# Performance work log

Measured on AMD Instinct MI355X. Metric: run time of the kernel, lower is better.

Reference implementation:

```python
import jax, jax.numpy as jnp
import numpy as np
from jax import lax

T, IMG, C_IN = 2048, 84, 4
HID = 256
NUM_OUT = 18
FEAT = 6 * 6 * 32  # 84 -> 42 -> 21 -> 11 -> 6 with stride-2 SAME convs


def setup_inputs() -> dict:
    key = jax.random.key(0)
    ks = jax.random.split(key, 8)
    d = {}
    d["x"] = jax.random.normal(ks[0], (T, IMG, IMG, C_IN), jnp.float32)
    cin = C_IN
    for i in range(4):
        d[f"conv_w{i}"] = jax.random.normal(ks[1 + i], (3, 3, cin, 32), jnp.float32) * (1.0 / np.sqrt(9 * cin))
        d[f"conv_b{i}"] = jnp.zeros((32,), jnp.float32)
        cin = 32
    d["lstm_w"] = jax.random.normal(ks[5], (FEAT + HID, 4 * HID), jnp.float32) * (1.0 / np.sqrt(FEAT + HID))
    d["lstm_b"] = jnp.zeros((4 * HID,), jnp.float32)
    d["fc_w"] = jax.random.normal(ks[6], (HID, NUM_OUT), jnp.float32) * 0.01
    d["fc_b"] = jnp.zeros((NUM_OUT,), jnp.float32)
    d["c_in"] = jnp.zeros((1, HID), jnp.float32)
    d["h_in"] = jnp.zeros((1, HID), jnp.float32)
    return d


def _conv_stack(x, ws, bs):
    dn = ("NHWC", "HWIO", "NHWC")
    for w, b in zip(ws, bs):
        x = jax.nn.elu(lax.conv_general_dilated(x, w, (2, 2), "SAME", dimension_numbers=dn) + b)
    return x.reshape(x.shape[0], -1)  # [T, FEAT]


def _lstm(feats, c0, h0, lstm_w, lstm_b):
    # BasicLSTMCell: gates [i, j, f, o], forget_bias = 1.0
    def step(carry, xt):
        c, h = carry  # [1, HID] each
        z = jnp.concatenate([xt[None, :], h], axis=1) @ lstm_w + lstm_b
        i, j, f, o = jnp.split(z, 4, axis=1)
        c = c * jax.nn.sigmoid(f + 1.0) + jax.nn.sigmoid(i) * jnp.tanh(j)
        h = jnp.tanh(c) * jax.nn.sigmoid(o)
        return (c, h), h[0]

    (_, _), hs = lax.scan(step, (c0, h0), feats)
    return hs  # [T, HID]


def reference(x, c_in, h_in,
              conv_w0, conv_b0, conv_w1, conv_b1,
              conv_w2, conv_b2, conv_w3, conv_b3,
              lstm_w, lstm_b, fc_w, fc_b):
    feats = _conv_stack(x, [conv_w0, conv_w1, conv_w2, conv_w3],
                        [conv_b0, conv_b1, conv_b2, conv_b3])
    hs = _lstm(feats, c_in, h_in, lstm_w, lstm_b)
    logits = hs @ fc_w + fc_b  # [T, NUM_OUT]
    return logits, hs
```

## Files before the change

### kernel.cpp

```cpp
#include <hip/hip_runtime.h>
#include <hip/hip_bf16.h>

__device__ inline float fsig(float x) { return 1.0f / (1.0f + __expf(-x)); }
__device__ inline float ftanh(float x) {
    float ax = fabsf(x);
    float e = __expf(-2.0f * ax);
    float r = (1.0f - e) / (1.0f + e);
    return x >= 0.0f ? r : -r;
}
__device__ inline float felu(float x) { return x > 0.0f ? x : expm1f(x); }

typedef _Float16 h2_t __attribute__((ext_vector_type(2)));

__device__ inline unsigned int packh2(float a, float b) {
    unsigned short ua = __builtin_bit_cast(unsigned short, (_Float16)a);
    unsigned short ub = __builtin_bit_cast(unsigned short, (_Float16)b);
    return (unsigned int)ua | ((unsigned int)ub << 16);
}
__device__ inline unsigned short f16bits(float a) {
    return __builtin_bit_cast(unsigned short, (_Float16)a);
}

__device__ inline float dot2acc(unsigned int w, unsigned int h, float acc) {
#if __has_builtin(__builtin_amdgcn_fdot2)
    return __builtin_amdgcn_fdot2(__builtin_bit_cast(h2_t, w), __builtin_bit_cast(h2_t, h), acc, false);
#else
    _Float16 wlo = __builtin_bit_cast(_Float16, (unsigned short)(w & 0xffff));
    _Float16 whi = __builtin_bit_cast(_Float16, (unsigned short)(w >> 16));
    _Float16 hlo = __builtin_bit_cast(_Float16, (unsigned short)(h & 0xffff));
    _Float16 hhi = __builtin_bit_cast(_Float16, (unsigned short)(h >> 16));
    return acc + (float)wlo * (float)hlo + (float)whi * (float)hhi;
#endif
}

__global__ __launch_bounds__(256) void conv0_kernel(const float* __restrict__ in,
                                                    const float* __restrict__ wg,
                                                    const float* __restrict__ bias,
                                                    unsigned short* __restrict__ out) {
    constexpr int W = 84, OW = 42, PAD = 0, WP = W + 2;
    __shared__ float in_s[3 * WP * 4];
    constexpr int NQ = 3 * WP;
    const int tid = threadIdx.x;
    const int oy = blockIdx.x;
    const int t = blockIdx.y;
    const int co = tid & 31;

    for (int q = tid; q < NQ; q += 256) {
        int ky = q / WP;
        int col = q - ky * WP;
        int iy = 2 * oy - PAD + ky;
        int ix = col - 1;
        float4 v = make_float4(0.f, 0.f, 0.f, 0.f);
        if (iy >= 0 && iy < W && ix >= 0 && ix < W)
            v = *(const float4*)&in[(((size_t)t * W + iy) * W + ix) * 4];
        *(float4*)&in_s[q * 4] = v;
    }

    float wr[9][4];
#pragma unroll
    for (int tap = 0; tap < 9; ++tap)
#pragma unroll
        for (int j = 0; j < 4; ++j) wr[tap][j] = wg[(tap * 4 + j) * 32 + co];
    __syncthreads();

    const int g = tid >> 5;
    constexpr int NOX = (OW + 7) / 8;
    float acc[NOX];
#pragma unroll
    for (int m = 0; m < NOX; ++m) acc[m] = 0.f;
#pragma unroll
    for (int ky = 0; ky < 3; ++ky)
#pragma unroll
        for (int kx = 0; kx < 3; ++kx) {
            float w0 = wr[ky * 3 + kx][0], w1 = wr[ky * 3 + kx][1];
            float w2 = wr[ky * 3 + kx][2], w3 = wr[ky * 3 + kx][3];
#pragma unroll
            for (int m = 0; m < NOX; ++m) {
                int ox = g + 8 * m;
                if (ox < OW) {
                    int cs = 2 * ox + kx - PAD + 1;
                    float4 xi = *(const float4*)&in_s[(ky * WP + cs) * 4];
                    acc[m] += xi.x * w0 + xi.y * w1 + xi.z * w2 + xi.w * w3;
                }
            }
        }
    float b = bias[co];
#pragma unroll
    for (int m = 0; m < NOX; ++m) {
        int ox = g + 8 * m;
        if (ox < OW)
            out[(((size_t)t * OW + oy) * OW + ox) * 32 + co] = f16bits(felu(acc[m] + b));
    }
}

template <int W, int OW, int PAD, bool F32OUT>
__global__ __launch_bounds__(256) void convh_kernel(const unsigned short* __restrict__ in,
                                                    const float* __restrict__ wg,
                                                    const float* __restrict__ bias,
                                                    void* __restrict__ outv) {
    constexpr int WP = W + 2;
    constexpr int OWH = (OW + 1) / 2;
    __shared__ __align__(16) unsigned short in_s[3][WP][32];
    __shared__ float zs[4][OW * 32];

    const int tid = threadIdx.x;
    const int oy = blockIdx.x;
    const int t = blockIdx.y;
    const int co = tid & 31;
    const int cig = (tid >> 5) & 3;
    const int oxh = tid >> 7;

    constexpr int NQ4 = 3 * WP * 4;
    uint4* in_s4 = reinterpret_cast<uint4*>(&in_s[0][0][0]);
    for (int q = tid; q < NQ4; q += 256) {
        int ky = q / (WP * 4);
        int rem = q - ky * (WP * 4);
        int col = rem >> 2, c4 = rem & 3;
        int iy = 2 * oy - PAD + ky;
        int ix = col - 1;
        uint4 v = make_uint4(0u, 0u, 0u, 0u);
        if (iy >= 0 && iy < W && ix >= 0 && ix < W)
            v = *(const uint4*)&in[(((size_t)t * W + iy) * W + ix) * 32 + c4 * 8];
        in_s4[q] = v;
    }

    unsigned int wr[9][4];
#pragma unroll
    for (int tap = 0; tap < 9; ++tap)
#pragma unroll
        for (int p = 0; p < 4; ++p)
            wr[tap][p] = packh2(wg[(tap * 32 + cig * 8 + 2 * p) * 32 + co],
                                wg[(tap * 32 + cig * 8 + 2 * p + 1) * 32 + co]);
    __syncthreads();

    float acc[OWH];
#pragma unroll
    for (int m = 0; m < OWH; ++m) acc[m] = 0.f;
#pragma unroll
    for (int ky = 0; ky < 3; ++ky)
#pragma unroll
        for (int kx = 0; kx < 3; ++kx) {
            unsigned int w0 = wr[ky * 3 + kx][0], w1 = wr[ky * 3 + kx][1];
            unsigned int w2 = wr[ky * 3 + kx][2], w3 = wr[ky * 3 + kx][3];
#pragma unroll
            for (int m = 0; m < OWH; ++m) {
                int ox = oxh * OWH + m;
                if (ox < OW) {
                    int cs = 2 * ox + kx - PAD + 1;
                    uint4 h8 = *(const uint4*)&in_s[ky][cs][cig * 8];
                    acc[m] = dot2acc(w0, h8.x, acc[m]);
                    acc[m] = dot2acc(w1, h8.y, acc[m]);
                    acc[m] = dot2acc(w2, h8.z, acc[m]);
                    acc[m] = dot2acc(w3, h8.w, acc[m]);
                }
            }
        }
#pragma unroll
    for (int m = 0; m < OWH; ++m) {
        int ox = oxh * OWH + m;
        if (ox < OW) zs[cig][ox * 32 + co] = acc[m];
    }
    __syncthreads();

    for (int idx = tid; idx < OW * 32; idx += 256) {
        float s = zs[0][idx] + zs[1][idx] + zs[2][idx] + zs[3][idx] + bias[idx & 31];
        s = felu(s);
        if constexpr (F32OUT)
            ((float*)outv)[(((size_t)t * OW + oy) * OW) * 32 + idx] = s;
        else
            ((unsigned short*)outv)[(((size_t)t * OW + oy) * OW) * 32 + idx] = f16bits(s);
    }
}

__global__ void gemm_kernel(const float* __restrict__ A, const float* __restrict__ Wx,
                            const float* __restrict__ bias, float* __restrict__ C) {
    __shared__ float As[32][64];
    __shared__ float Bs[32][64];
    const int bn = blockIdx.x, bm = blockIdx.y;
    const int tx = threadIdx.x, ty = threadIdx.y;
    const int tid = ty * 16 + tx;
    float acc[4][4] = {};
    for (int k0 = 0; k0 < 1152; k0 += 32) {
        {
            int r = tid >> 3;
            int c = (tid & 7) * 4;
            float4 a0 = *(const float4*)&A[(size_t)(bm * 64 + r) * 1152 + k0 + c];
            float4 a1 = *(const float4*)&A[(size_t)(bm * 64 + r + 32) * 1152 + k0 + c];
            As[c + 0][r] = a0.x; As[c + 1][r] = a0.y; As[c + 2][r] = a0.z; As[c + 3][r] = a0.w;
            As[c + 0][r + 32] = a1.x; As[c + 1][r + 32] = a1.y; As[c + 2][r + 32] = a1.z; As[c + 3][r + 32] = a1.w;
            int rb = tid >> 4;
            int cb = (tid & 15) * 4;
            *(float4*)&Bs[rb][cb] = *(const float4*)&Wx[(size_t)(k0 + rb) * 1024 + bn * 64 + cb];
            *(float4*)&Bs[rb + 16][cb] = *(const float4*)&Wx[(size_t)(k0 + rb + 16) * 1024 + bn * 64 + cb];
        }
        __syncthreads();
#pragma unroll
        for (int kk = 0; kk < 32; ++kk) {
            float4 a = *(float4*)&As[kk][ty * 4];
            float4 b = *(float4*)&Bs[kk][tx * 4];
            acc[0][0] += a.x * b.x; acc[0][1] += a.x * b.y; acc[0][2] += a.x * b.z; acc[0][3] += a.x * b.w;
            acc[1][0] += a.y * b.x; acc[1][1] += a.y * b.y; acc[1][2] += a.y * b.z; acc[1][3] += a.y * b.w;
            acc[2][0] += a.z * b.x; acc[2][1] += a.z * b.y; acc[2][2] += a.z * b.z; acc[2][3] += a.z * b.w;
            acc[3][0] += a.w * b.x; acc[3][1] += a.w * b.y; acc[3][2] += a.w * b.z; acc[3][3] += a.w * b.w;
        }
        __syncthreads();
    }
#pragma unroll
    for (int i = 0; i < 4; ++i) {
        int row = bm * 64 + ty * 4 + i;
#pragma unroll
        for (int j = 0; j < 4; ++j) {
            int col = bn * 64 + tx * 4 + j;
            C[(size_t)row * 1024 + col] = acc[i][j] + bias[col];
        }
    }
}

__global__ __attribute__((amdgpu_flat_work_group_size(512, 512), amdgpu_num_vgpr(256)))
void lstm7_kernel(const float* __restrict__ lstm_w,
                  const float* __restrict__ xpart,
                  const float* __restrict__ c_in,
                  const float* __restrict__ h_in,
                  float* __restrict__ hs_out) {
    __shared__ __align__(16) unsigned int wl[512][52];
    __shared__ float zsm[2][4][256];
    __shared__ __align__(16) unsigned int hpk[2][2][68];

    const int tid = threadIdx.x;
    const int s = tid >> 8;
    const int u = tid & 255;

    for (int q = 0; q < 4; ++q)
        for (int p = 0; p < 12; ++p) {
            int gp = 64 * s + p;
            wl[tid][q * 12 + p] = packh2(lstm_w[(size_t)(1152 + 2 * gp) * 1024 + 256 * q + u],
                                         lstm_w[(size_t)(1152 + 2 * gp + 1) * 1024 + 256 * q + u]);
        }
    unsigned int wreg[4][52];
#pragma unroll
    for (int q = 0; q < 4; ++q)
        for (int p = 12; p < 64; ++p) {
            int gp = 64 * s + p;
            wreg[q][p - 12] = packh2(lstm_w[(size_t)(1152 + 2 * gp) * 1024 + 256 * q + u],
                                     lstm_w[(size_t)(1152 + 2 * gp + 1) * 1024 + 256 * q + u]);
        }

    float c_state = c_in[u];
    if (tid < 256) {
        unsigned short* hrow = (unsigned short*)&hpk[0][u >> 7][0];
        hrow[u & 127] = f16bits(h_in[u]);
    }
    __syncthreads();

    float xp0 = xpart[u], xp1 = xpart[256 + u], xp2 = xpart[512 + u], xp3 = xpart[768 + u];

    for (int t = 0; t < 2048; ++t) {
        const int cur = t & 1;
        const uint4* hq = reinterpret_cast<const uint4*>(&hpk[cur][s][0]);

        float acc[4] = {0.f, 0.f, 0.f, 0.f};
        {
            uint4 hA = hq[0], hB = hq[1], hC = hq[2];
#pragma unroll
            for (int q = 0; q < 4; ++q) {
                uint4 wa = *(const uint4*)&wl[tid][q * 12];
                uint4 wb = *(const uint4*)&wl[tid][q * 12 + 4];
                uint4 wc = *(const uint4*)&wl[tid][q * 12 + 8];
                acc[q] = dot2acc(wa.x, hA.x, acc[q]); acc[q] = dot2acc(wa.y, hA.y, acc[q]);
                acc[q] = dot2acc(wa.z, hA.z, acc[q]); acc[q] = dot2acc(wa.w, hA.w, acc[q]);
                acc[q] = dot2acc(wb.x, hB.x, acc[q]); acc[q] = dot2acc(wb.y, hB.y, acc[q]);
                acc[q] = dot2acc(wb.z, hB.z, acc[q]); acc[q] = dot2acc(wb.w, hB.w, acc[q]);
                acc[q] = dot2acc(wc.x, hC.x, acc[q]); acc[q] = dot2acc(wc.y, hC.y, acc[q]);
                acc[q] = dot2acc(wc.z, hC.z, acc[q]); acc[q] = dot2acc(wc.w, hC.w, acc[q]);
            }
        }
#pragma unroll
        for (int c = 3; c < 16; ++c) {
            uint4 h4 = hq[c];
            const int r = 4 * (c - 3);
#pragma unroll
            for (int q = 0; q < 4; ++q) {
                acc[q] = dot2acc(wreg[q][r + 0], h4.x, acc[q]);
                acc[q] = dot2acc(wreg[q][r + 1], h4.y, acc[q]);
                acc[q] = dot2acc(wreg[q][r + 2], h4.z, acc[q]);
                acc[q] = dot2acc(wreg[q][r + 3], h4.w, acc[q]);
            }
        }
        zsm[s][0][u] = acc[0];
        zsm[s][1][u] = acc[1];
        zsm[s][2][u] = acc[2];
        zsm[s][3][u] = acc[3];

        float xn0 = 0.f, xn1 = 0.f, xn2 = 0.f, xn3 = 0.f;
        if (t + 1 < 2048) {
            const float* xr = &xpart[(size_t)(t + 1) * 1024];
            xn0 = xr[u]; xn1 = xr[256 + u]; xn2 = xr[512 + u]; xn3 = xr[768 + u];
        }

        asm volatile("s_waitcnt lgkmcnt(0)\n\ts_barrier" ::: "memory");

        float zi = zsm[0][0][u] + zsm[1][0][u] + xp0;
        float zj = zsm[0][1][u] + zsm[1][1][u] + xp1;
        float zf = zsm[0][2][u] + zsm[1][2][u] + xp2;
        float zo = zsm[0][3][u] + zsm[1][3][u] + xp3;
        c_state = c_state * fsig(zf + 1.0f) + fsig(zi) * ftanh(zj);
        float h = ftanh(c_state) * fsig(zo);
        if (tid < 256) {
            hs_out[(size_t)t * 256 + u] = h;
            unsigned short* hrow = (unsigned short*)&hpk[cur ^ 1][u >> 7][0];
            hrow[u & 127] = f16bits(h);
        }

        asm volatile("s_waitcnt lgkmcnt(0)\n\ts_barrier" ::: "memory");
        xp0 = xn0; xp1 = xn1; xp2 = xn2; xp3 = xn3;
    }
}

__global__ void logits_kernel(const float* __restrict__ hs, const float* __restrict__ fc_w,
                              const float* __restrict__ fc_b, float* __restrict__ out) {
    int idx = blockIdx.x * 256 + threadIdx.x;
    if (idx >= 2048 * 18) return;
    int t = idx / 18, n = idx % 18;
    float acc = fc_b[n];
    const float* hrow = hs + (size_t)t * 256;
#pragma unroll 4
    for (int k = 0; k < 256; ++k) acc += hrow[k] * fc_w[k * 18 + n];
    out[idx] = acc;
}

extern "C" void kernel_launch(void* const* d_in, const int* in_sizes, int n_in,
                              void* d_out, int out_size, void* d_ws, size_t ws_size,
                              hipStream_t stream) {
    const float* x   = (const float*)d_in[0];
    const float* w0  = (const float*)d_in[1];
    const float* b0  = (const float*)d_in[2];
    const float* w1  = (const float*)d_in[3];
    const float* b1  = (const float*)d_in[4];
    const float* w2  = (const float*)d_in[5];
    const float* b2  = (const float*)d_in[6];
    const float* w3  = (const float*)d_in[7];
    const float* b3  = (const float*)d_in[8];
    const float* lw  = (const float*)d_in[9];
    const float* lb  = (const float*)d_in[10];
    const float* fcw = (const float*)d_in[11];
    const float* fcb = (const float*)d_in[12];
    const float* cin = (const float*)d_in[13];
    const float* hin = (const float*)d_in[14];

    float* outp = (float*)d_out;
    float* hs_out = outp + 2048 * 18;

    const size_t FIXED_B = ((size_t)2048 * 1152 + (size_t)2048 * 1024) * 4;
    const size_t PERT_B = ((size_t)56448 + 14112 + 3872) * 2;

    int C = 128;
    const int cands[5] = {2048, 1024, 512, 256, 128};
    for (int i = 0; i < 5; ++i) {
        if (FIXED_B + (size_t)cands[i] * PERT_B <= ws_size) { C = cands[i]; break; }
    }

    float* feats = (float*)d_ws;
    float* xpart = feats + (size_t)2048 * 1152;
    unsigned short* c0buf = (unsigned short*)(xpart + (size_t)2048 * 1024);
    unsigned short* c1buf = c0buf + (size_t)C * 56448;
    unsigned short* c2buf = c1buf + (size_t)C * 14112;

    for (int t0 = 0; t0 < 2048; t0 += C) {
        const float* xin = x + (size_t)t0 * 84 * 84 * 4;
        conv0_kernel<<<dim3(42, C), 256, 0, stream>>>(xin, w0, b0, c0buf);
        convh_kernel<42, 21, 0, false><<<dim3(21, C), 256, 0, stream>>>(c0buf, w1, b1, c1buf);
        convh_kernel<21, 11, 1, false><<<dim3(11, C), 256, 0, stream>>>(c1buf, w2, b2, c2buf);
        convh_kernel<11, 6, 1, true><<<dim3(6, C), 256, 0, stream>>>(c2buf, w3, b3,
                                                                     feats + (size_t)t0 * 1152);
    }

    gemm_kernel<<<dim3(16, 32), dim3(16, 16), 0, stream>>>(feats, lw, lb, xpart);
    lstm7_kernel<<<1, 512, 0, stream>>>(lw, xpart, cin, hin, hs_out);
    logits_kernel<<<144, 256, 0, stream>>>(hs_out, fcw, fcb, outp);
}
```

Before: 4.262 ms.

## Reduce LSTM split-K halves via intra-wave shuffle, drop one barrier per step

The single-block LSTM kernel now maps the two K-halves for each hidden unit to the two 32-lane halves of one wavefront instead of two separate 256-thread groups. Partial gate sums are combined with a cross-lane xor shuffle rather than a shared-memory buffer, so the first block-wide barrier and the zsm round-trip are removed from every timestep. This targets the serial per-step latency of the 2048-step recurrence. In exchange, the hidden-state buffer layout and weight distribution change, and the launch-bounds attribute replaces the explicit VGPR cap, which may change register allocation for the large register-resident weight array.

After: 4.337 ms. Within noise of the previous version (+1.8%).

```diff
diff --git a/kernel.cpp b/kernel.cpp
--- a/kernel.cpp
+++ b/kernel.cpp
@@ -216,99 +216,113 @@
     }
 }
 
-__global__ __attribute__((amdgpu_flat_work_group_size(512, 512), amdgpu_num_vgpr(256)))
-void lstm7_kernel(const float* __restrict__ lstm_w,
-                  const float* __restrict__ xpart,
-                  const float* __restrict__ c_in,
-                  const float* __restrict__ h_in,
-                  float* __restrict__ hs_out) {
+__global__ __launch_bounds__(512) void lstm9_kernel(const float* __restrict__ lstm_w,
+                                                    const float* __restrict__ xpart,
+                                                    const float* __restrict__ c_in,
+                                                    const float* __restrict__ h_in,
+                                                    float* __restrict__ hs_out) {
     __shared__ __align__(16) unsigned int wl[512][52];
-    __shared__ float zsm[2][4][256];
-    __shared__ __align__(16) unsigned int hpk[2][2][68];
+    __shared__ __align__(16) unsigned short hpk[2][256];
 
     const int tid = threadIdx.x;
-    const int s = tid >> 8;
-    const int u = tid & 255;
+    const int wv = tid >> 6;
+    const int l = tid & 63;
+    const int s = l >> 5;
+    const int u0 = (wv << 5) + (l & 31);
 
     for (int q = 0; q < 4; ++q)
-        for (int p = 0; p < 12; ++p) {
-            int gp = 64 * s + p;
-            wl[tid][q * 12 + p] = packh2(lstm_w[(size_t)(1152 + 2 * gp) * 1024 + 256 * q + u],
-                                         lstm_w[(size_t)(1152 + 2 * gp + 1) * 1024 + 256 * q + u]);
-        }
+        for (int p = 0; p < 12; ++p)
+            wl[tid][q * 12 + p] = packh2(
+                lstm_w[(size_t)(1152 + 128 * s + 2 * p) * 1024 + (q << 8) + u0],
+                lstm_w[(size_t)(1152 + 128 * s + 2 * p + 1) * 1024 + (q << 8) + u0]);
     unsigned int wreg[4][52];
 #pragma unroll
     for (int q = 0; q < 4; ++q)
-        for (int p = 12; p < 64; ++p) {
-            int gp = 64 * s + p;
-            wreg[q][p - 12] = packh2(lstm_w[(size_t)(1152 + 2 * gp) * 1024 + 256 * q + u],
-                                     lstm_w[(size_t)(1152 + 2 * gp + 1) * 1024 + 256 * q + u]);
-        }
-
-    float c_state = c_in[u];
-    if (tid < 256) {
-        unsigned short* hrow = (unsigned short*)&hpk[0][u >> 7][0];
-        hrow[u & 127] = f16bits(h_in[u]);
-    }
+        for (int p = 12; p < 64; ++p)
+            wreg[q][p - 12] = packh2(
+                lstm_w[(size_t)(1152 + 128 * s + 2 * p) * 1024 + (q << 8) + u0],
+                lstm_w[(size_t)(1152 + 128 * s + 2 * p + 1) * 1024 + (q << 8) + u0]);
+
+    float c_state = c_in[u0];
+    if (tid < 256) hpk[0][tid] = f16bits(h_in[tid]);
     __syncthreads();
 
-    float xp0 = xpart[u], xp1 = xpart[256 + u], xp2 = xpart[512 + u], xp3 = xpart[768 + u];
+    float xp0 = xpart[u0], xp1 = xpart[256 + u0], xp2 = xpart[512 + u0], xp3 = xpart[768 + u0];
 
     for (int t = 0; t < 2048; ++t) {
         const int cur = t & 1;
-        const uint4* hq = reinterpret_cast<const uint4*>(&hpk[cur][s][0]);
-
-        float acc[4] = {0.f, 0.f, 0.f, 0.f};
+        const uint4* hq = reinterpret_cast<const uint4*>(&hpk[cur][s << 7]);
+
+        float a0 = 0.f, a1 = 0.f, a2 = 0.f, a3 = 0.f;
         {
             uint4 hA = hq[0], hB = hq[1], hC = hq[2];
-#pragma unroll
-            for (int q = 0; q < 4; ++q) {
-                uint4 wa = *(const uint4*)&wl[tid][q * 12];
-                uint4 wb = *(const uint4*)&wl[tid][q * 12 + 4];
-                uint4 wc = *(const uint4*)&wl[tid][q * 12 + 8];
-                acc[q] = dot2acc(wa.x, hA.x, acc[q]); acc[q] = dot2acc(wa.y, hA.y, acc[q]);
-                acc[q] = dot2acc(wa.z, hA.z, acc[q]); acc[q] = dot2acc(wa.w, hA.w, acc[q]);
-                acc[q] = dot2acc(wb.x, hB.x, acc[q]); acc[q] = dot2acc(wb.y, hB.y, acc[q]);
-                acc[q] = dot2acc(wb.z, hB.z, acc[q]); acc[q] = dot2acc(wb.w, hB.w, acc[q]);
-                acc[q] = dot2acc(wc.x, hC.x, acc[q]); acc[q] = dot2acc(wc.y, hC.y, acc[q]);
-                acc[q] = dot2acc(wc.z, hC.z, acc[q]); acc[q] = dot2acc(wc.w, hC.w, acc[q]);
-            }
+            uint4 w0a = *(const uint4*)&wl[tid][0];
+            uint4 w0b = *(const uint4*)&wl[tid][4];
+            uint4 w0c = *(const uint4*)&wl[tid][8];
+            a0 = dot2acc(w0a.x, hA.x, a0); a0 = dot2acc(w0a.y, hA.y, a0);
+            a0 = dot2acc(w0a.z, hA.z, a0); a0 = dot2acc(w0a.w, hA.w, a0);
+            a0 = dot2acc(w0b.x, hB.x, a0); a0 = dot2acc(w0b.y, hB.y, a0);
+            a0 = dot2acc(w0b.z, hB.z, a0); a0 = dot2acc(w0b.w, hB.w, a0);
+            a0 = dot2acc(w0c.x, hC.x, a0); a0 = dot2acc(w0c.y, hC.y, a0);
+            a0 = dot2acc(w0c.z, hC.z, a0); a0 = dot2acc(w0c.w, hC.w, a0);
+            uint4 w1a = *(const uint4*)&wl[tid][12];
+            uint4 w1b = *(const uint4*)&wl[tid][16];
+            uint4 w1c = *(const uint4*)&wl[tid][20];
+            a1 = dot2acc(w1a.x, hA.x, a1); a1 = dot2acc(w1a.y, hA.y, a1);
+            a1 = dot2acc(w1a.z, hA.z, a1); a1 = dot2acc(w1a.w, hA.w, a1);
+            a1 = dot2acc(w1b.x, hB.x, a1); a1 = dot2acc(w1b.y, hB.y, a1);
+            a1 = dot2acc(w1b.z, hB.z, a1); a1 = dot2acc(w1b.w, hB.w, a1);
+            a1 = dot2acc(w1c.x, hC.x, a1); a1 = dot2acc(w1c.y, hC.y, a1);
+            a1 = dot2acc(w1c.z, hC.z, a1); a1 = dot2acc(w1c.w, hC.w, a1);
+            uint4 w2a = *(const uint4*)&wl[tid][24];
+            uint4 w2b = *(const uint4*)&wl[tid][28];
+            uint4 w2c = *(const uint4*)&wl[tid][32];
+            a2 = dot2acc(w2a.x, hA.x, a2); a2 = dot2acc(w2a.y, hA.y, a2);
+            a2 = dot2acc(w2a.z, hA.z, a2); a2 = dot2acc(w2a.w, hA.w, a2);
+            a2 = dot2acc(w2b.x, hB.x, a2); a2 = dot2acc(w2b.y, hB.y, a2);
+            a2 = dot2acc(w2b.z, hB.z, a2); a2 = dot2acc(w2b.w, hB.w, a2);
+            a2 = dot2acc(w2c.x, hC.x, a2); a2 = dot2acc(w2c.y, hC.y, a2);
+            a2 = dot2acc(w2c.z, hC.z, a2); a2 = dot2acc(w2c.w, hC.w, a2);
+            uint4 w3a = *(const uint4*)&wl[tid][36];
+            uint4 w3b = *(const uint4*)&wl[tid][40];
+            uint4 w3c = *(const uint4*)&wl[tid][44];
+            a3 = dot2acc(w3a.x, hA.x, a3); a3 = dot2acc(w3a.y, hA.y, a3);
+            a3 = dot2acc(w3a.z, hA.z, a3); a3 = dot2acc(w3a.w, hA.w, a3);
+            a3 = dot2acc(w3b.x, hB.x, a3); a3 = dot2acc(w3b.y, hB.y, a3);
+            a3 = dot2acc(w3b.z, hB.z, a3); a3 = dot2acc(w3b.w, hB.w, a3);
+            a3 = dot2acc(w3c.x, hC.x, a3); a3 = dot2acc(w3c.y, hC.y, a3);
+            a3 = dot2acc(w3c.z, hC.z, a3); a3 = dot2acc(w3c.w, hC.w, a3);
         }
 #pragma unroll
         for (int c = 3; c < 16; ++c) {
             uint4 h4 = hq[c];
             const int r = 4 * (c - 3);
-#pragma unroll
-            for (int q = 0; q < 4; ++q) {
-                acc[q] = dot2acc(wreg[q][r + 0], h4.x, acc[q]);
-                acc[q] = dot2acc(wreg[q][r + 1], h4.y, acc[q]);
-                acc[q] = dot2acc(wreg[q][r + 2], h4.z, acc[q]);
-                acc[q] = dot2acc(wreg[q][r + 3], h4.w, acc[q]);
-            }
-        }
-        zsm[s][0][u] = acc[0];
-        zsm[s][1][u] = acc[1];
-        zsm[s][2][u] = acc[2];
-        zsm[s][3][u] = acc[3];
+            a0 = dot2acc(wreg[0][r + 0], h4.x, a0); a0 = dot2acc(wreg[0][r + 1], h4.y, a0);
+            a0 = dot2acc(wreg[0][r + 2], h4.z, a0); a0 = dot2acc(wreg[0][r + 3], h4.w, a0);
+            a1 = dot2acc(wreg[1][r + 0], h4.x, a1); a1 = dot2acc(wreg[1][r + 1], h4.y, a1);
+            a1 = dot2acc(wreg[1][r + 2], h4.z, a1); a1 = dot2acc(wreg[1][r + 3], h4.w, a1);
+            a2 = dot2acc(wreg[2][r + 0], h4.x, a2); a2 = dot2acc(wreg[2][r + 1], h4.y, a2);
+            a2 = dot2acc(wreg[2][r + 2], h4.z, a2); a2 = dot2acc(wreg[2][r + 3], h4.w, a2);
+            a3 = dot2acc(wreg[3][r + 0], h4.x, a3); a3 = dot2acc(wreg[3][r + 1], h4.y, a3);
+            a3 = dot2acc(wreg[3][r + 2], h4.z, a3); a3 = dot2acc(wreg[3][r + 3], h4.w, a3);
+        }
 
         float xn0 = 0.f, xn1 = 0.f, xn2 = 0.f, xn3 = 0.f;
         if (t + 1 < 2048) {
             const float* xr = &xpart[(size_t)(t + 1) * 1024];
-            xn0 = xr[u]; xn1 = xr[256 + u]; xn2 = xr[512 + u]; xn3 = xr[768 + u];
-        }
-
-        asm volatile("s_waitcnt lgkmcnt(0)\n\ts_barrier" ::: "memory");
-
-        float zi = zsm[0][0][u] + zsm[1][0][u] + xp0;
-        float zj = zsm[0][1][u] + zsm[1][1][u] + xp1;
-        float zf = zsm[0][2][u] + zsm[1][2][u] + xp2;
-        float zo = zsm[0][3][u] + zsm[1][3][u] + xp3;
+            xn0 = xr[u0]; xn1 = xr[256 + u0]; xn2 = xr[512 + u0]; xn3 = xr[768 + u0];
+        }
+
+        float zi = a0 + __shfl_xor(a0, 32, 64) + xp0;
+        float zj = a1 + __shfl_xor(a1, 32, 64) + xp1;
+        float zf = a2 + __shfl_xor(a2, 32, 64) + xp2;
+        float zo = a3 + __shfl_xor(a3, 32, 64) + xp3;
+
         c_state = c_state * fsig(zf + 1.0f) + fsig(zi) * ftanh(zj);
         float h = ftanh(c_state) * fsig(zo);
-        if (tid < 256) {
-            hs_out[(size_t)t * 256 + u] = h;
-            unsigned short* hrow = (unsigned short*)&hpk[cur ^ 1][u >> 7][0];
-            hrow[u & 127] = f16bits(h);
+        if (s == 0) {
+            hs_out[(size_t)t * 256 + u0] = h;
+            hpk[cur ^ 1][u0] = f16bits(h);
         }
 
         asm volatile("s_waitcnt lgkmcnt(0)\n\ts_barrier" ::: "memory");
@@ -375,6 +389,6 @@
     }
 
     gemm_kernel<<<dim3(16, 32), dim3(16, 16), 0, stream>>>(feats, lw, lb, xpart);
-    lstm7_kernel<<<1, 512, 0, stream>>>(lw, xpart, cin, hin, hs_out);
+    lstm9_kernel<<<1, 512, 0, stream>>>(lw, xpart, cin, hin, hs_out);
     logits_kernel<<<144, 256, 0, stream>>>(hs_out, fcw, fcb, outp);
 }
```
